# Performance work log

Hardware: AMD Instinct MI355X
Metric: run time of the kernel (lower is better)

Reference implementation:

```python
import jax, jax.numpy as jnp
import numpy as np

N, C, H, W = 2, 32, 128, 256
MAX_DISP = 48


def setup_inputs() -> dict:
    key = jax.random.key(0)
    k1, k2 = jax.random.split(key)
    l_fmap = jax.random.normal(k1, (N, C, H, W), dtype=jnp.float32)
    r_fmap = jax.random.normal(k2, (N, C, H, W), dtype=jnp.float32)
    return {"l_fmap": l_fmap, "r_fmap": r_fmap}


def reference(l_fmap, r_fmap):
    # Faithful to make_cost_volume_naive: cost[:, :, d, :, d:] = l[..., d:] - r[..., :-d],
    # positions w < d keep the init value 1.0. Fully vectorized over disparity.
    n, c, h, w = l_fmap.shape
    d_idx = jnp.arange(MAX_DISP)[:, None]          # [D,1]
    w_idx = jnp.arange(w)[None, :]                 # [1,W]
    src = jnp.clip(w_idx - d_idx, 0, w - 1)        # [D,W] gather index into r's width
    # r shifted right by d per disparity: [N,C,H,D,W] -> [N,C,D,H,W]
    r_shift = jnp.moveaxis(r_fmap[:, :, :, src], 3, 2)
    mask = (w_idx >= d_idx)[None, None, :, None, :]  # [1,1,D,1,W]
    cost = jnp.where(mask, l_fmap[:, :, None, :, :] - r_shift, jnp.float32(1.0))
    return cost  # [N,C,D,H,W]
```

## Files before the change

kernel.cpp:

```cpp
#include <hip/hip_runtime.h>

constexpr int N = 2, C = 32, H = 128, W = 256, D = 48;
constexpr int NC = N * C;
constexpr int W4 = W / 4;
constexpr int PASSES = D / 4;

__global__ __launch_bounds__(256) void cost_volume_kernel(
    const float* __restrict__ l,
    const float* __restrict__ r,
    float4* __restrict__ out)
{
    __shared__ float r_lds[D + W];

    const int blk = blockIdx.x;
    const int h   = blk & (H - 1);
    const int nc  = blk >> 7;

    const float* lrow = l + (size_t)blk * W;
    const float* rrow = r + (size_t)blk * W;

    const int t = threadIdx.x;
    r_lds[D + t] = rrow[t];
    if (t < D) r_lds[t] = 0.0f;

    const int lane = t & 63;
    const int wv   = t >> 6;
    const int w0   = lane << 2;

    const float4 lv = *reinterpret_cast<const float4*>(lrow + w0);

    __syncthreads();

    float4* obase = out + (((size_t)nc * D * H) + h) * W4 + lane;
    const size_t dstride = (size_t)H * W4;

    #pragma unroll
    for (int pass = 0; pass < PASSES; ++pass) {
        const int d = wv + pass * 4;
        const float* rs = r_lds + (D - d) + w0;
        float4 o;
        o.x = (w0 + 0 >= d) ? lv.x - rs[0] : 1.0f;
        o.y = (w0 + 1 >= d) ? lv.y - rs[1] : 1.0f;
        o.z = (w0 + 2 >= d) ? lv.z - rs[2] : 1.0f;
        o.w = (w0 + 3 >= d) ? lv.w - rs[3] : 1.0f;
        obase[(size_t)d * dstride] = o;
    }
}

extern "C" void kernel_launch(void* const* d_in, const int* in_sizes, int n_in,
                              void* d_out, int out_size, void* d_ws, size_t ws_size,
                              hipStream_t stream)
{
    const float* l = (const float*)d_in[0];
    const float* r = (const float*)d_in[1];
    float4* out = (float4*)d_out;

    constexpr int GRID = NC * H;
    cost_volume_kernel<<<GRID, 256, 0, stream>>>(l, r, out);
}
```

Measured before the change: 404.2 us.

## Assign one disparity plane per block with contiguous nontemporal stores

Changes the work split from one block per (n,c,h) row writing 48 scattered disparity planes to one block per (n,c,d) plane that streams a contiguous 128-row region. The shifted right operand is built by reading two neighbouring float4 values from global memory and selecting lanes via a template on d mod 4, which removes the LDS staging and the barrier. Output uses nontemporal stores to avoid polluting the cache with the write-only volume. Inputs are now re-read 48 times per (n,c), relying on cache hits.

```diff
diff --git a/kernel.cpp b/kernel.cpp
--- a/kernel.cpp
+++ b/kernel.cpp
@@ -3,47 +3,65 @@
 constexpr int N = 2, C = 32, H = 128, W = 256, D = 48;
 constexpr int NC = N * C;
 constexpr int W4 = W / 4;
-constexpr int PASSES = D / 4;
+
+typedef float f32x4 __attribute__((ext_vector_type(4)));
+
+template <int S>
+__device__ __forceinline__ void plane_loop(const f32x4* __restrict__ l4,
+                                           const f32x4* __restrict__ r4,
+                                           f32x4* __restrict__ o4,
+                                           int q, int d, int lane, int wv)
+{
+    const int rvi = max(lane - q, 0);
+    const int rmi = max(lane - q - 1, 0);
+    const int w0  = lane << 2;
+
+    #pragma unroll 4
+    for (int h = wv; h < H; h += 4) {
+        const int row = h * W4;
+        const f32x4 lv = l4[row + lane];
+        const f32x4 rv = r4[row + rvi];
+        f32x4 rm = rv;
+        if (S != 0) rm = r4[row + rmi];
+
+        float rs0, rs1, rs2, rs3;
+        if (S == 0) { rs0 = rv.x; rs1 = rv.y; rs2 = rv.z; rs3 = rv.w; }
+        if (S == 1) { rs0 = rm.w; rs1 = rv.x; rs2 = rv.y; rs3 = rv.z; }
+        if (S == 2) { rs0 = rm.z; rs1 = rm.w; rs2 = rv.x; rs3 = rv.y; }
+        if (S == 3) { rs0 = rm.y; rs1 = rm.z; rs2 = rm.w; rs3 = rv.x; }
+
+        f32x4 o;
+        o.x = (w0 + 0 >= d) ? lv.x - rs0 : 1.0f;
+        o.y = (w0 + 1 >= d) ? lv.y - rs1 : 1.0f;
+        o.z = (w0 + 2 >= d) ? lv.z - rs2 : 1.0f;
+        o.w = (w0 + 3 >= d) ? lv.w - rs3 : 1.0f;
+
+        __builtin_nontemporal_store(o, &o4[row + lane]);
+    }
+}
 
 __global__ __launch_bounds__(256) void cost_volume_kernel(
     const float* __restrict__ l,
     const float* __restrict__ r,
-    float4* __restrict__ out)
+    f32x4* __restrict__ out)
 {
-    __shared__ float r_lds[D + W];
-
-    const int blk = blockIdx.x;
-    const int h   = blk & (H - 1);
-    const int nc  = blk >> 7;
-
-    const float* lrow = l + (size_t)blk * W;
-    const float* rrow = r + (size_t)blk * W;
-
-    const int t = threadIdx.x;
-    r_lds[D + t] = rrow[t];
-    if (t < D) r_lds[t] = 0.0f;
-
+    const int blk  = blockIdx.x;
+    const int d    = blk % D;
+    const int nc   = blk / D;
+    const int t    = threadIdx.x;
     const int lane = t & 63;
     const int wv   = t >> 6;
-    const int w0   = lane << 2;
 
-    const float4 lv = *reinterpret_cast<const float4*>(lrow + w0);
+    const f32x4* l4 = reinterpret_cast<const f32x4*>(l) + (size_t)nc * H * W4;
+    const f32x4* r4 = reinterpret_cast<const f32x4*>(r) + (size_t)nc * H * W4;
+    f32x4* o4 = out + (size_t)blk * H * W4;
 
-    __syncthreads();
-
-    float4* obase = out + (((size_t)nc * D * H) + h) * W4 + lane;
-    const size_t dstride = (size_t)H * W4;
-
-    #pragma unroll
-    for (int pass = 0; pass < PASSES; ++pass) {
-        const int d = wv + pass * 4;
-        const float* rs = r_lds + (D - d) + w0;
-        float4 o;
-        o.x = (w0 + 0 >= d) ? lv.x - rs[0] : 1.0f;
-        o.y = (w0 + 1 >= d) ? lv.y - rs[1] : 1.0f;
-        o.z = (w0 + 2 >= d) ? lv.z - rs[2] : 1.0f;
-        o.w = (w0 + 3 >= d) ? lv.w - rs[3] : 1.0f;
-        obase[(size_t)d * dstride] = o;
+    const int q = d >> 2;
+    switch (d & 3) {
+        case 0: plane_loop<0>(l4, r4, o4, q, d, lane, wv); break;
+        case 1: plane_loop<1>(l4, r4, o4, q, d, lane, wv); break;
+        case 2: plane_loop<2>(l4, r4, o4, q, d, lane, wv); break;
+        case 3: plane_loop<3>(l4, r4, o4, q, d, lane, wv); break;
     }
 }
 
@@ -53,8 +71,8 @@
 {
     const float* l = (const float*)d_in[0];
     const float* r = (const float*)d_in[1];
-    float4* out = (float4*)d_out;
+    f32x4* out = (f32x4*)d_out;
 
-    constexpr int GRID = NC * H;
+    constexpr int GRID = NC * D;
     cost_volume_kernel<<<GRID, 256, 0, stream>>>(l, r, out);
 }
```

Result: slower. 441.4 us (+9.2%).
